# Performance work log

Measured on AMD Instinct MI355X. Metric: run time of the kernel, lower is better.

Reference implementation:

```python
import jax, jax.numpy as jnp
import numpy as np
import math

N_HEADS = 16
D_MODEL = 1024
D_FF = 4096
MAX_REL = 32  # max_relative_position
LN_EPS = 1e-5


def _layernorm(x, g, b):
    m = jnp.mean(x, axis=-1, keepdims=True)
    v = jnp.var(x, axis=-1, keepdims=True)
    return (x - m) * jax.lax.rsqrt(v + LN_EPS) * g + b


def setup_inputs() -> dict:
    key = jax.random.key(0)
    ks = jax.random.split(key, 12)
    D, F = D_MODEL, D_FF
    gain = 1.0 / math.sqrt(2.0)
    xav = lambda k, o, i, g=1.0: jax.random.uniform(k, (o, i), jnp.float32, -1.0, 1.0) * (g * math.sqrt(6.0 / (o + i)))
    return {
        "x": jax.random.normal(ks[0], (2, 2048, D), jnp.float32),
        "wq": xav(ks[1], D, D, gain),
        "wk": xav(ks[2], D, D, gain),
        "wv": xav(ks[3], D, D, gain),
        "wo": xav(ks[4], D, D, gain),
        "wo_b": jnp.zeros((D,), jnp.float32),
        "rel_tab": jax.random.normal(ks[5], (2 * MAX_REL - 1, N_HEADS), jnp.float32) * 0.02,
        "ln1_g": jnp.ones((D,), jnp.float32),
        "ln1_b": jnp.zeros((D,), jnp.float32),
        "ln2_g": jnp.ones((D,), jnp.float32),
        "ln2_b": jnp.zeros((D,), jnp.float32),
        "w1": xav(ks[6], F, D),
        "b1": jnp.zeros((F,), jnp.float32),
        "w2": xav(ks[7], D, F),
        "b2": jnp.zeros((D,), jnp.float32),
    }


def reference(x, wq, wk, wv, wo, wo_b, rel_tab, ln1_g, ln1_b, ln2_g, ln2_b, w1, b1, w2, b2):
    B, S, D = x.shape
    H = N_HEADS
    dk = D // H

    def proj(w):  # torch Linear: x @ w.T, then split heads -> [B,H,S,dk]
        return (x @ w.T).reshape(B, S, H, dk).transpose(0, 2, 1, 3)

    q, k, v = proj(wq), proj(wk), proj(wv)

    # Rotary embeddings (per-head dim), exact interleave-to-block formula from source
    t = jnp.arange(S, dtype=jnp.float32)
    inv_freq = 1.0 / (10000.0 ** (jnp.arange(0, dk, 2, dtype=jnp.float32) / dk))
    freqs = t[:, None] * inv_freq[None, :]  # [S, dk/2]
    cos, sin = jnp.cos(freqs), jnp.sin(freqs)

    def rope(z):
        z1, z2 = z[..., ::2], z[..., 1::2]  # [B,H,S,dk/2]
        return jnp.concatenate([z1 * cos - z2 * sin, z1 * sin + z2 * cos], axis=-1)

    q, k = rope(q), rope(k)

    # Manual attention with learned relative-position bias
    scores = jnp.einsum("bhqd,bhkd->bhqk", q, k) / math.sqrt(dk)
    rel = jnp.arange(S)[:, None] - jnp.arange(S)[None, :]
    rel = jnp.clip(rel, -(MAX_REL - 1), MAX_REL - 1) + (MAX_REL - 1)
    bias = rel_tab[rel]  # [S,S,H]
    scores = scores + jnp.transpose(bias, (2, 0, 1))[None]  # [1,H,S,S]
    attn = jax.nn.softmax(scores, axis=-1)
    o = jnp.einsum("bhqk,bhkd->bhqd", attn, v).transpose(0, 2, 1, 3).reshape(B, S, D)
    o = o @ wo.T + wo_b

    # Post-norm residual block
    h = _layernorm(x + o, ln1_g, ln1_b)
    f = jax.nn.gelu(h @ w1.T + b1, approximate=False) @ w2.T + b2
    return _layernorm(h + f, ln2_g, ln2_b)
```

## Files before the change

### kernel.cpp

```cpp
#include <hip/hip_runtime.h>
#include <stdint.h>

#define MB (1ull << 20)
typedef unsigned short u16;
typedef __attribute__((ext_vector_type(8))) short bf16x8;
typedef __attribute__((ext_vector_type(4))) float f32x4;

__device__ __forceinline__ float b2f(u16 u) {
  union { unsigned int i; float f; } c; c.i = ((unsigned int)u) << 16; return c.f;
}
__device__ __forceinline__ u16 f2b(float f) {
  union { float f; unsigned int i; } c; c.f = f;
  unsigned int r = c.i + 0x7fffu + ((c.i >> 16) & 1u);
  return (u16)(r >> 16);
}
__device__ __forceinline__ void gload16(const void* g, void* l) {
  __builtin_amdgcn_global_load_lds(
      (const __attribute__((address_space(1))) void*)g,
      (__attribute__((address_space(3))) void*)l, 16, 0, 0);
}

__global__ __launch_bounds__(256) void f2b_all(
    const float* __restrict__ x, const float* __restrict__ wq, const float* __restrict__ wk,
    const float* __restrict__ wv, const float* __restrict__ wo, const float* __restrict__ w1,
    const float* __restrict__ w2,
    u16* __restrict__ xb, u16* __restrict__ wqkvb, u16* __restrict__ wob,
    u16* __restrict__ w1b, u16* __restrict__ w2b)
{
  int bid = blockIdx.x;
  const float* src; u16* dst;
  if (bid < 4096)       { src = x;  dst = xb; }
  else if (bid < 5120)  { src = wq; dst = wqkvb;           bid -= 4096; }
  else if (bid < 6144)  { src = wk; dst = wqkvb + 1048576; bid -= 5120; }
  else if (bid < 7168)  { src = wv; dst = wqkvb + 2097152; bid -= 6144; }
  else if (bid < 8192)  { src = wo; dst = wob;             bid -= 7168; }
  else if (bid < 12288) { src = w1; dst = w1b;             bid -= 8192; }
  else                  { src = w2; dst = w2b;             bid -= 12288; }
  int i = (bid * 256 + threadIdx.x) * 4;
  float4 v = *(const float4*)(src + i);
  uint2 ov;
  ov.x = (unsigned)f2b(v.x) | ((unsigned)f2b(v.y) << 16);
  ov.y = (unsigned)f2b(v.z) | ((unsigned)f2b(v.w) << 16);
  *(uint2*)(dst + i) = ov;
}

__global__ __launch_bounds__(256) void rope_tab_kernel(float2* __restrict__ tab) {
  int idx = blockIdx.x * 256 + threadIdx.x;
  int s = idx >> 5, j = idx & 31;
  float inv = exp2f(-(float)j * (13.287712379549449f / 32.0f));
  float sn, cs;
  sincosf((float)s * inv, &sn, &cs);
  tab[idx] = make_float2(cs, sn);
}

template<int EPI, int BM>
__global__ __launch_bounds__(256) void gemm_bt(
    const u16* __restrict__ A, const u16* __restrict__ B,
    u16* __restrict__ C, const float* __restrict__ bias,
    int M, int N, int K)
{
  constexpr int MT = BM / 32;
  __shared__ __align__(16) u16 As[BM * 64];
  __shared__ __align__(16) u16 Bs[128 * 64];
  const int tid = threadIdx.x;
  const int lane = tid & 63, wave = tid >> 6;
  const int lr = lane & 15, lg = lane >> 4;
  const int wm = wave >> 1, wn = wave & 1;

  const int nwg = gridDim.x * gridDim.y;
  const int id = blockIdx.y * gridDim.x + blockIdx.x;
  const int nid = (id & 7) * (nwg >> 3) + (id >> 3);
  const int bx = nid % gridDim.x, by = nid / gridDim.x;

  const int srow = tid >> 3;
  const int scsw = ((tid & 7) * 8) ^ ((srow & 7) << 3);
  const size_t abase = (size_t)(by * BM + srow) * K + scsw;
  const size_t bbase = (size_t)(bx * 128 + srow) * K + scsw;

  int aoff[MT][2], boff[4][2];
  #pragma unroll
  for (int mt = 0; mt < MT; mt++) {
    int row = wm * (BM / 2) + mt * 16 + lr;
    #pragma unroll
    for (int kk = 0; kk < 2; kk++)
      aoff[mt][kk] = row * 64 + ((kk * 32 + lg * 8) ^ ((row & 7) << 3));
  }
  #pragma unroll
  for (int nt = 0; nt < 4; nt++) {
    int row = wn * 64 + nt * 16 + lr;
    #pragma unroll
    for (int kk = 0; kk < 2; kk++)
      boff[nt][kk] = row * 64 + ((kk * 32 + lg * 8) ^ ((row & 7) << 3));
  }

  f32x4 acc[MT][4];
  #pragma unroll
  for (int i = 0; i < MT; i++)
    #pragma unroll
    for (int j = 0; j < 4; j++) acc[i][j] = (f32x4){0.f, 0.f, 0.f, 0.f};

  for (int k0 = 0; k0 < K; k0 += 64) {
    __syncthreads();
    #pragma unroll
    for (int h = 0; h < MT; h++)
      gload16(A + abase + (size_t)(h * 32) * K + k0, &As[h * 2048 + tid * 8]);
    #pragma unroll
    for (int h = 0; h < 4; h++)
      gload16(B + bbase + (size_t)(h * 32) * K + k0, &Bs[h * 2048 + tid * 8]);
    __syncthreads();
    #pragma unroll
    for (int kk = 0; kk < 2; kk++) {
      bf16x8 af[MT], bfr[4];
      #pragma unroll
      for (int mt = 0; mt < MT; mt++) af[mt] = *(const bf16x8*)&As[aoff[mt][kk]];
      #pragma unroll
      for (int nt = 0; nt < 4; nt++) bfr[nt] = *(const bf16x8*)&Bs[boff[nt][kk]];
      #pragma unroll
      for (int mt = 0; mt < MT; mt++)
        #pragma unroll
        for (int nt = 0; nt < 4; nt++)
          acc[mt][nt] = __builtin_amdgcn_mfma_f32_16x16x32_bf16(af[mt], bfr[nt], acc[mt][nt], 0, 0, 0);
    }
  }

  #pragma unroll
  for (int mt = 0; mt < MT; mt++)
    #pragma unroll
    for (int nt = 0; nt < 4; nt++) {
      const int row = by * BM + wm * (BM / 2) + mt * 16 + lg * 4;
      const int col = bx * 128 + wn * 64 + nt * 16 + lr;
      const float bv = (EPI >= 1) ? bias[col] : 0.f;
      #pragma unroll
      for (int r = 0; r < 4; r++) {
        float x = acc[mt][nt][r] + bv;
        if (EPI == 2) x = 0.5f * x * (1.f + erff(x * 0.70710678118654752f));
        C[(size_t)(row + r) * N + col] = f2b(x);
      }
    }
}

#define MFMA16(BASE, BF)                                                       \
  __builtin_amdgcn_s_setprio(1);                                               \
  _Pragma("unroll")                                                            \
  for (int mt = 0; mt < 4; mt++)                                               \
    _Pragma("unroll")                                                          \
    for (int nt = 0; nt < 4; nt++)                                             \
      acc[(BASE) + mt][nt] = __builtin_amdgcn_mfma_f32_16x16x32_bf16(          \
          af[mt], BF[nt], acc[(BASE) + mt][nt], 0, 0, 0);                      \
  __builtin_amdgcn_s_setprio(0);

#define SA2(bb, eta, kb)                                                             \
  gload16(Ab + ((size_t)(eta) * 128) * K + (kb), &As[bb][eta][tid * 8]);             \
  gload16(Ab + ((size_t)(eta) * 128 + 64) * K + (kb), &As[bb][eta][4096 + tid * 8]);
#define SB2(bb, eta, kb)                                                             \
  gload16(Bb + ((size_t)(eta) * 128) * K + (kb), &Bs[bb][eta][tid * 8]);             \
  gload16(Bb + ((size_t)(eta) * 128 + 64) * K + (kb), &Bs[bb][eta][4096 + tid * 8]);

#define SBAR asm volatile("s_barrier" ::: "memory")

template<int EPI>
__global__ __launch_bounds__(512) void gemm256(
    const u16* __restrict__ A, const u16* __restrict__ B,
    u16* __restrict__ C, const float* __restrict__ bias,
    int M, int N, int K)
{
  __shared__ __align__(16) u16 As[2][2][8192];
  __shared__ __align__(16) u16 Bs[2][2][8192];
  const int tid = threadIdx.x;
  const int lane = tid & 63, wave = tid >> 6;
  const int lr = lane & 15, lg = lane >> 4;
  const int wm = wave >> 2, wn = wave & 3;

  const int nwg = gridDim.x * gridDim.y;
  const int id = blockIdx.y * gridDim.x + blockIdx.x;
  const int nid = (id & 7) * (nwg >> 3) + (id >> 3);
  const int bx = nid % gridDim.x, by = nid / gridDim.x;

  const int srow = tid >> 3;
  const int scsw = ((tid & 7) * 8) ^ ((srow & 7) << 3);
  const u16* Ab = A + (size_t)(by * 256 + srow) * K + scsw;
  const u16* Bb = B + (size_t)(bx * 256 + srow) * K + scsw;

  int aoff[2][2][4], boff[2][4];
  #pragma unroll
  for (int mh = 0; mh < 2; mh++)
    #pragma unroll
    for (int kk = 0; kk < 2; kk++)
      #pragma unroll
      for (int mt = 0; mt < 4; mt++) {
        int row = mh * 64 + mt * 16 + lr;
        aoff[mh][kk][mt] = row * 64 + ((kk * 32 + lg * 8) ^ ((lr & 7) << 3));
      }
  #pragma unroll
  for (int kk = 0; kk < 2; kk++)
    #pragma unroll
    for (int nt = 0; nt < 4; nt++) {
      int row = (wn & 1) * 64 + nt * 16 + lr;
      boff[kk][nt] = row * 64 + ((kk * 32 + lg * 8) ^ ((lr & 7) << 3));
    }

  f32x4 acc[8][4];
  #pragma unroll
  for (int i = 0; i < 8; i++)
    #pragma unroll
    for (int j = 0; j < 4; j++) acc[i][j] = (f32x4){0.f, 0.f, 0.f, 0.f};

  const int NT = K >> 6;

  SB2(0, 0, 0) SB2(0, 1, 0) SA2(0, 0, 0) SA2(0, 1, 0)

  for (int t = 0; t < NT; ++t) {
    const int c = t & 1, n = c ^ 1;
    const size_t kb = (size_t)(t + 1) * 64;
    const bool st = (t + 1 < NT);
    const u16* Ac = As[c][wm];
    const u16* Bc = Bs[c][wn >> 1];
    bf16x8 b0[4], b1[4], af[4];

    asm volatile("s_waitcnt vmcnt(0)" ::: "memory");
    SBAR;
    #pragma unroll
    for (int nt = 0; nt < 4; nt++) b0[nt] = *(const bf16x8*)&Bc[boff[0][nt]];
    #pragma unroll
    for (int mt = 0; mt < 4; mt++) af[mt] = *(const bf16x8*)&Ac[aoff[0][0][mt]];
    if (st) { SB2(n, 0, kb) }
    MFMA16(0, b0)
    SBAR;
    #pragma unroll
    for (int nt = 0; nt < 4; nt++) b1[nt] = *(const bf16x8*)&Bc[boff[1][nt]];
    #pragma unroll
    for (int mt = 0; mt < 4; mt++) af[mt] = *(const bf16x8*)&Ac[aoff[0][1][mt]];
    if (st) { SA2(n, 0, kb) }
    SBAR;
    MFMA16(0, b1)
    SBAR;
    #pragma unroll
    for (int mt = 0; mt < 4; mt++) af[mt] = *(const bf16x8*)&Ac[aoff[1][0][mt]];
    if (st) { SB2(n, 1, kb) }
    SBAR;
    MFMA16(4, b0)
    SBAR;
    #pragma unroll
    for (int mt = 0; mt < 4; mt++) af[mt] = *(const bf16x8*)&Ac[aoff[1][1][mt]];
    if (st) { SA2(n, 1, kb) }
    SBAR;
    MFMA16(4, b1)
    SBAR;
  }

  #pragma unroll
  for (int m8 = 0; m8 < 8; m8++)
    #pragma unroll
    for (int nt = 0; nt < 4; nt++) {
      const int row = by * 256 + wm * 128 + m8 * 16 + lg * 4;
      const int col = bx * 256 + wn * 64 + nt * 16 + lr;
      const float bv = (EPI >= 1) ? bias[col] : 0.f;
      #pragma unroll
      for (int r = 0; r < 4; r++) {
        float x = acc[m8][nt][r] + bv;
        if (EPI == 2) x = 0.5f * x * (1.f + erff(x * 0.70710678118654752f));
        C[(size_t)(row + r) * N + col] = f2b(x);
      }
    }
}

__global__ __launch_bounds__(256) void rope_kernel(
    const u16* __restrict__ qp, const u16* __restrict__ kp, int stride,
    const float2* __restrict__ tab, u16* __restrict__ qr, u16* __restrict__ kr)
{
  const int gid = blockIdx.x * 4 + (threadIdx.x >> 6);
  const int lane = threadIdx.x & 63;
  const int s = gid & 2047;
  const int bh = gid >> 11;
  const int h = bh & 15, b = bh >> 4;
  const int j = lane & 31;
  float2 t = tab[s * 32 + j];
  const float cs = t.x, sn = t.y;
  const size_t base = (size_t)(b * 2048 + s) * stride + h * 64;
  unsigned int qv = *(const unsigned int*)(qp + base + 2 * j);
  unsigned int kv = *(const unsigned int*)(kp + base + 2 * j);
  float q1 = b2f((u16)qv), q2 = b2f((u16)(qv >> 16));
  float k1 = b2f((u16)kv), k2 = b2f((u16)(kv >> 16));
  float qo = (lane < 32) ? (q1 * cs - q2 * sn) : (q1 * sn + q2 * cs);
  float ko = (lane < 32) ? (k1 * cs - k2 * sn) : (k1 * sn + k2 * cs);
  qr[(size_t)gid * 64 + lane] = f2b(qo * 0.18033688011112042f);
  kr[(size_t)gid * 64 + lane] = f2b(ko);
}

__global__ __launch_bounds__(256) void vtrans_kernel(
    const u16* __restrict__ vp, int stride, u16* __restrict__ vT)
{
  __shared__ u16 t[64][65];
  const int sc = blockIdx.x & 31;
  const int bh = blockIdx.x >> 5;
  const int h = bh & 15, b = bh >> 4;
  const int tid = threadIdx.x;
  #pragma unroll
  for (int i = 0; i < 16; i++) {
    int idx = i * 256 + tid;
    int sl = idx >> 6, d = idx & 63;
    t[sl][d] = vp[(size_t)(b * 2048 + sc * 64 + sl) * stride + h * 64 + d];
  }
  __syncthreads();
  #pragma unroll
  for (int i = 0; i < 16; i++) {
    int idx = i * 256 + tid;
    int d = idx >> 6, sl = idx & 63;
    vT[((size_t)bh * 64 + d) * 2048 + sc * 64 + sl] = t[sl][d];
  }
}

__global__ __launch_bounds__(256) void attn_kernel(
    const u16* __restrict__ qr, const u16* __restrict__ kr,
    const u16* __restrict__ vT, const float* __restrict__ rel_tab,
    u16* __restrict__ o)
{
  __shared__ __align__(16) u16 Ks[2][64 * 64];
  __shared__ __align__(16) u16 Vs[2][64 * 64];
  __shared__ float bias_s[64];

  const int tid = threadIdx.x;
  const int lane = tid & 63, wave = tid >> 6;
  const int lr = lane & 15, lg = lane >> 4;

  const int id = blockIdx.x;
  const int nid = (id & 7) * 128 + (id >> 3);
  const int bh = nid >> 5, qc = nid & 31;
  const int h = bh & 15, b = bh >> 4;
  const int q0 = qc * 64 + wave * 16;

  if (tid < 63) bias_s[tid] = rel_tab[tid * 16 + h] * 1.4426950408889634f;

  const u16* qb = qr + (size_t)bh * 2048 * 64;
  const u16* kb = kr + (size_t)bh * 2048 * 64;
  const u16* vb = vT + (size_t)bh * 64 * 2048;

  bf16x8 qf[2];
  qf[0] = *(const bf16x8*)(qb + (size_t)(q0 + lr) * 64 + lg * 8);
  qf[1] = *(const bf16x8*)(qb + (size_t)(q0 + lr) * 64 + 32 + lg * 8);

  const int srow = tid >> 3;
  const int scsw = ((tid & 7) * 8) ^ ((srow & 7) << 3);

  int koff[4][2];
  #pragma unroll
  for (int nt = 0; nt < 4; nt++)
    #pragma unroll
    for (int ks = 0; ks < 2; ks++)
      koff[nt][ks] = (nt * 16 + lr) * 64 + ((ks * 32 + lg * 8) ^ ((lr & 7) << 3));

  #pragma unroll
  for (int hh = 0; hh < 2; hh++) {
    gload16(kb + (size_t)(hh * 32 + srow) * 64 + scsw, &Ks[0][hh * 2048 + tid * 8]);
    gload16(vb + (size_t)(hh * 32 + srow) * 2048 + scsw, &Vs[0][hh * 2048 + tid * 8]);
  }

  float mrow = -1e30f;
  f32x4 lvec = (f32x4){0.f, 0.f, 0.f, 0.f};
  f32x4 oacc[4];
  #pragma unroll
  for (int nt = 0; nt < 4; nt++) oacc[nt] = (f32x4){0.f, 0.f, 0.f, 0.f};

  const int idx_lo = 4 * (lr + 16 * ((lg & 1) * 2));
  const int idx_hi = idx_lo + 64;
  const bool hiSel = (lg >= 2);

  int cur = 0;
  for (int kc = 0; kc < 32; kc++) {
    const int k0 = kc * 64;
    __syncthreads();
    if (kc < 31) {
      const int kn = k0 + 64;
      #pragma unroll
      for (int hh = 0; hh < 2; hh++) {
        gload16(kb + (size_t)(kn + hh * 32 + srow) * 64 + scsw, &Ks[cur ^ 1][hh * 2048 + tid * 8]);
        gload16(vb + (size_t)(hh * 32 + srow) * 2048 + kn + scsw, &Vs[cur ^ 1][hh * 2048 + tid * 8]);
      }
    }
    const u16* Kc = Ks[cur];
    const u16* Vc = Vs[cur];

    f32x4 sacc[4];
    #pragma unroll
    for (int nt = 0; nt < 4; nt++) sacc[nt] = (f32x4){0.f, 0.f, 0.f, 0.f};
    __builtin_amdgcn_s_setprio(1);
    #pragma unroll
    for (int ks = 0; ks < 2; ks++)
      #pragma unroll
      for (int nt = 0; nt < 4; nt++) {
        bf16x8 kf = *(const bf16x8*)&Kc[koff[nt][ks]];
        sacc[nt] = __builtin_amdgcn_mfma_f32_16x16x32_bf16(kf, qf[ks], sacc[nt], 0, 0, 0);
      }
    __builtin_amdgcn_s_setprio(0);

    f32x4 pvv[4];
    const int dmin = q0 - k0 - 63, dmax = q0 + 15 - k0;
    if (dmin >= 31 || dmax <= -31) {
      const float c = bias_s[dmin >= 31 ? 62 : 0];
      f32x4 m4;
      #pragma unroll
      for (int i = 0; i < 4; i++)
        m4[i] = fmaxf(fmaxf(sacc[0][i], sacc[1][i]), fmaxf(sacc[2][i], sacc[3][i]));
      float rm = fmaxf(fmaxf(m4[0], m4[1]), fmaxf(m4[2], m4[3])) + c;
      rm = fmaxf(rm, __shfl_xor(rm, 16));
      rm = fmaxf(rm, __shfl_xor(rm, 32));
      if (!__all(rm <= mrow + 11.5f)) {
        float mnew = fmaxf(mrow, rm);
        float sc = exp2f(mrow - mnew);
        lvec *= sc;
        #pragma unroll
        for (int nt = 0; nt < 4; nt++) oacc[nt] *= sc;
        mrow = mnew;
      }
      const float off = c - mrow;
      #pragma unroll
      for (int nt = 0; nt < 4; nt++) pvv[nt] = sacc[nt] + off;
    } else {
      #pragma unroll
      for (int nt = 0; nt < 4; nt++)
        #pragma unroll
        for (int r = 0; r < 4; r++) {
          int d = (q0 + lr) - (k0 + nt * 16 + lg * 4 + r);
          d = d < -31 ? -31 : (d > 31 ? 31 : d);
          pvv[nt][r] = sacc[nt][r] + bias_s[d + 31];
        }
      f32x4 m4;
      #pragma unroll
      for (int i = 0; i < 4; i++)
        m4[i] = fmaxf(fmaxf(pvv[0][i], pvv[1][i]), fmaxf(pvv[2][i], pvv[3][i]));
      float rm = fmaxf(fmaxf(m4[0], m4[1]), fmaxf(m4[2], m4[3]));
      rm = fmaxf(rm, __shfl_xor(rm, 16));
      rm = fmaxf(rm, __shfl_xor(rm, 32));
      if (!__all(rm <= mrow + 11.5f)) {
        float mnew = fmaxf(mrow, rm);
        float sc = exp2f(mrow - mnew);
        lvec *= sc;
        #pragma unroll
        for (int nt = 0; nt < 4; nt++) oacc[nt] *= sc;
        mrow = mnew;
      }
      #pragma unroll
      for (int nt = 0; nt < 4; nt++) pvv[nt] = pvv[nt] - mrow;
    }

    unsigned int pk[4][2];
    #pragma unroll
    for (int nt = 0; nt < 4; nt++) {
      f32x4 p;
      #pragma unroll
      for (int i = 0; i < 4; i++) p[i] = exp2f(pvv[nt][i]);
      lvec += p;
      unsigned int pr0, pr1;
      asm("v_cvt_pk_bf16_f32 %0, %1, %2" : "=v"(pr0) : "v"(p[0]), "v"(p[1]));
      asm("v_cvt_pk_bf16_f32 %0, %1, %2" : "=v"(pr1) : "v"(p[2]), "v"(p[3]));
      pk[nt][0] = pr0;
      pk[nt][1] = pr1;
    }

    __builtin_amdgcn_s_setprio(1);
    #pragma unroll
    for (int ks = 0; ks < 2; ks++) {
      int w0a = __builtin_amdgcn_ds_bpermute(idx_lo, (int)pk[ks * 2][0]);
      int w0b = __builtin_amdgcn_ds_bpermute(idx_lo, (int)pk[ks * 2 + 1][0]);
      int w1a = __builtin_amdgcn_ds_bpermute(idx_lo, (int)pk[ks * 2][1]);
      int w1b = __builtin_amdgcn_ds_bpermute(idx_lo, (int)pk[ks * 2 + 1][1]);
      int w2a = __builtin_amdgcn_ds_bpermute(idx_hi, (int)pk[ks * 2][0]);
      int w2b = __builtin_amdgcn_ds_bpermute(idx_hi, (int)pk[ks * 2 + 1][0]);
      int w3a = __builtin_amdgcn_ds_bpermute(idx_hi, (int)pk[ks * 2][1]);
      int w3b = __builtin_amdgcn_ds_bpermute(idx_hi, (int)pk[ks * 2 + 1][1]);
      int4 bw;
      bw.x = hiSel ? w0b : w0a;
      bw.y = hiSel ? w1b : w1a;
      bw.z = hiSel ? w2b : w2a;
      bw.w = hiSel ? w3b : w3a;
      bf16x8 pf = *(bf16x8*)&bw;
      #pragma unroll
      for (int nt = 0; nt < 4; nt++) {
        bf16x8 vf = *(const bf16x8*)&Vc[koff[nt][ks]];
        oacc[nt] = __builtin_amdgcn_mfma_f32_16x16x32_bf16(vf, pf, oacc[nt], 0, 0, 0);
      }
    }
    __builtin_amdgcn_s_setprio(0);
    cur ^= 1;
  }

  float lpart = (lvec[0] + lvec[1]) + (lvec[2] + lvec[3]);
  lpart += __shfl_xor(lpart, 16);
  lpart += __shfl_xor(lpart, 32);
  const float inv = 1.0f / lpart;
  const size_t obase = (size_t)(b * 2048 + q0 + lr) * 1024 + h * 64;
  #pragma unroll
  for (int nt = 0; nt < 4; nt++) {
    uint2 st;
    st.x = (unsigned)f2b(oacc[nt][0] * inv) | ((unsigned)f2b(oacc[nt][1] * inv) << 16);
    st.y = (unsigned)f2b(oacc[nt][2] * inv) | ((unsigned)f2b(oacc[nt][3] * inv) << 16);
    *(uint2*)(o + obase + nt * 16 + lg * 4) = st;
  }
}

__global__ __launch_bounds__(256) void ln1_kernel(
    const float* __restrict__ x, const u16* __restrict__ ao,
    const float* __restrict__ g, const float* __restrict__ bta,
    u16* __restrict__ hb)
{
  const int row = blockIdx.x, tid = threadIdx.x;
  const int wave = tid >> 6, lane = tid & 63;
  const int c = tid * 4;
  float4 xv = *(const float4*)(x + (size_t)row * 1024 + c);
  uint2 av = *(const uint2*)(ao + (size_t)row * 1024 + c);
  float v0 = xv.x + b2f((u16)av.x);
  float v1 = xv.y + b2f((u16)(av.x >> 16));
  float v2 = xv.z + b2f((u16)av.y);
  float v3 = xv.w + b2f((u16)(av.y >> 16));
  float s = (v0 + v1) + (v2 + v3);
  float s2 = (v0 * v0 + v1 * v1) + (v2 * v2 + v3 * v3);
  #pragma unroll
  for (int off = 32; off >= 1; off >>= 1) { s += __shfl_down(s, off); s2 += __shfl_down(s2, off); }
  __shared__ float rs[4], rs2[4];
  if (lane == 0) { rs[wave] = s; rs2[wave] = s2; }
  __syncthreads();
  s = rs[0] + rs[1] + rs[2] + rs[3];
  s2 = rs2[0] + rs2[1] + rs2[2] + rs2[3];
  float mean = s * (1.f / 1024.f);
  float var = s2 * (1.f / 1024.f) - mean * mean;
  float inv = rsqrtf(var + 1e-5f);
  float4 gv = *(const float4*)(g + c);
  float4 bv = *(const float4*)(bta + c);
  uint2 ov;
  ov.x = (unsigned)f2b((v0 - mean) * inv * gv.x + bv.x) |
         ((unsigned)f2b((v1 - mean) * inv * gv.y + bv.y) << 16);
  ov.y = (unsigned)f2b((v2 - mean) * inv * gv.z + bv.z) |
         ((unsigned)f2b((v3 - mean) * inv * gv.w + bv.w) << 16);
  *(uint2*)(hb + (size_t)row * 1024 + c) = ov;
}

__global__ __launch_bounds__(256) void ln2_kernel(
    const u16* __restrict__ hb, const u16* __restrict__ fb,
    const float* __restrict__ g, const float* __restrict__ bta,
    float* __restrict__ out)
{
  const int row = blockIdx.x, tid = threadIdx.x;
  const int wave = tid >> 6, lane = tid & 63;
  const int c = tid * 4;
  uint2 hv = *(const uint2*)(hb + (size_t)row * 1024 + c);
  uint2 fv = *(const uint2*)(fb + (size_t)row * 1024 + c);
  float v0 = b2f((u16)hv.x) + b2f((u16)fv.x);
  float v1 = b2f((u16)(hv.x >> 16)) + b2f((u16)(fv.x >> 16));
  float v2 = b2f((u16)hv.y) + b2f((u16)fv.y);
  float v3 = b2f((u16)(hv.y >> 16)) + b2f((u16)(fv.y >> 16));
  float s = (v0 + v1) + (v2 + v3);
  float s2 = (v0 * v0 + v1 * v1) + (v2 * v2 + v3 * v3);
  #pragma unroll
  for (int off = 32; off >= 1; off >>= 1) { s += __shfl_down(s, off); s2 += __shfl_down(s2, off); }
  __shared__ float rs[4], rs2[4];
  if (lane == 0) { rs[wave] = s; rs2[wave] = s2; }
  __syncthreads();
  s = rs[0] + rs[1] + rs[2] + rs[3];
  s2 = rs2[0] + rs2[1] + rs2[2] + rs2[3];
  float mean = s * (1.f / 1024.f);
  float var = s2 * (1.f / 1024.f) - mean * mean;
  float inv = rsqrtf(var + 1e-5f);
  float4 gv = *(const float4*)(g + c);
  float4 bv = *(const float4*)(bta + c);
  float4 ov;
  ov.x = (v0 - mean) * inv * gv.x + bv.x;
  ov.y = (v1 - mean) * inv * gv.y + bv.y;
  ov.z = (v2 - mean) * inv * gv.z + bv.z;
  ov.w = (v3 - mean) * inv * gv.w + bv.w;
  *(float4*)(out + (size_t)row * 1024 + c) = ov;
}

extern "C" void kernel_launch(void* const* d_in, const int* in_sizes, int n_in,
                              void* d_out, int out_size, void* d_ws, size_t ws_size,
                              hipStream_t stream)
{
  const float* x    = (const float*)d_in[0];
  const float* wq   = (const float*)d_in[1];
  const float* wk   = (const float*)d_in[2];
  const float* wv   = (const float*)d_in[3];
  const float* wo   = (const float*)d_in[4];
  const float* wo_b = (const float*)d_in[5];
  const float* rel  = (const float*)d_in[6];
  const float* ln1g = (const float*)d_in[7];
  const float* ln1b = (const float*)d_in[8];
  const float* ln2g = (const float*)d_in[9];
  const float* ln2b = (const float*)d_in[10];
  const float* w1   = (const float*)d_in[11];
  const float* b1   = (const float*)d_in[12];
  const float* w2   = (const float*)d_in[13];
  const float* b2   = (const float*)d_in[14];
  float* out = (float*)d_out;
  char* w = (char*)d_ws;

  if (ws_size < (size_t)90 * MB) return;

  u16* xb    = (u16*)(w + 0 * MB);
  u16* wqkvb = (u16*)(w + 8 * MB);
  u16* wob   = (u16*)(w + 14 * MB);
  u16* w1b   = (u16*)(w + 16 * MB);
  u16* w2b   = (u16*)(w + 24 * MB);
  u16* qkv   = (u16*)(w + 32 * MB);
  u16* ob    = (u16*)(w + 32 * MB);
  u16* ao    = (u16*)(w + 40 * MB);
  u16* hb    = (u16*)(w + 48 * MB);
  u16* qrb   = (u16*)(w + 56 * MB);
  u16* krb   = (u16*)(w + 64 * MB);
  u16* vTb   = (u16*)(w + 72 * MB);
  u16* gb    = (u16*)(w + 56 * MB);
  u16* fb    = (u16*)(w + 0 * MB);
  float2* tab = (float2*)(w + 88 * MB);

  const int M = 4096, D = 1024, F = 4096;

  rope_tab_kernel<<<dim3(256), 256, 0, stream>>>(tab);
  f2b_all<<<dim3(16384), 256, 0, stream>>>(x, wq, wk, wv, wo, w1, w2,
                                           xb, wqkvb, wob, w1b, w2b);

  gemm256<0><<<dim3(3 * D / 256, M / 256), 512, 0, stream>>>(xb, wqkvb, qkv, nullptr, M, 3 * D, D);

  rope_kernel<<<dim3(16384), 256, 0, stream>>>(qkv, qkv + 1024, 3 * D, tab, qrb, krb);
  vtrans_kernel<<<dim3(1024), 256, 0, stream>>>(qkv + 2048, 3 * D, vTb);

  attn_kernel<<<dim3(1024), 256, 0, stream>>>(qrb, krb, vTb, rel, ob);

  gemm_bt<1, 64><<<dim3(D / 128, M / 64), 256, 0, stream>>>(ob, wob, ao, wo_b, M, D, D);

  ln1_kernel<<<dim3(M), 256, 0, stream>>>(x, ao, ln1g, ln1b, hb);

  gemm256<2><<<dim3(F / 256, M / 256), 512, 0, stream>>>(hb, w1b, gb, b1, M, F, D);

  gemm_bt<1, 64><<<dim3(D / 128, M / 64), 256, 0, stream>>>(gb, w2b, fb, b2, M, D, F);

  ln2_kernel<<<dim3(M), 256, 0, stream>>>(hb, fb, ln2g, ln2b, out);
}
```

Measured before the change: 289.6 us.

## Process two 16-row query tiles per wave in attention to reuse K/V tiles

Each attention block now handles 128 query rows instead of 64: every wave keeps two independent Q fragments and two sets of softmax state and accumulators. Each K/V tile loaded into LDS then feeds twice as many MFMAs, and the grid shrinks from 1024 to 512 blocks. This halves global K/V traffic and LDS fill per query and gives more independent MFMA work to interleave. The cost is roughly double the accumulator registers, which may lower occupancy, and 512 blocks may underfill the GPU's compute units.

Result: slower. 298.0 us (+2.9%).

```diff
diff --git a/kernel.cpp b/kernel.cpp
--- a/kernel.cpp
+++ b/kernel.cpp
@@ -324,10 +324,11 @@
   const int lr = lane & 15, lg = lane >> 4;
 
   const int id = blockIdx.x;
-  const int nid = (id & 7) * 128 + (id >> 3);
-  const int bh = nid >> 5, qc = nid & 31;
+  const int nid = (id & 7) * 64 + (id >> 3);
+  const int bh = nid >> 4, qc = nid & 15;
   const int h = bh & 15, b = bh >> 4;
-  const int q0 = qc * 64 + wave * 16;
+  const int q0a = qc * 128 + wave * 16;
+  const int q0b = q0a + 64;
 
   if (tid < 63) bias_s[tid] = rel_tab[tid * 16 + h] * 1.4426950408889634f;
 
@@ -335,9 +336,11 @@
   const u16* kb = kr + (size_t)bh * 2048 * 64;
   const u16* vb = vT + (size_t)bh * 64 * 2048;
 
-  bf16x8 qf[2];
-  qf[0] = *(const bf16x8*)(qb + (size_t)(q0 + lr) * 64 + lg * 8);
-  qf[1] = *(const bf16x8*)(qb + (size_t)(q0 + lr) * 64 + 32 + lg * 8);
+  bf16x8 qfa[2], qfb[2];
+  qfa[0] = *(const bf16x8*)(qb + (size_t)(q0a + lr) * 64 + lg * 8);
+  qfa[1] = *(const bf16x8*)(qb + (size_t)(q0a + lr) * 64 + 32 + lg * 8);
+  qfb[0] = *(const bf16x8*)(qb + (size_t)(q0b + lr) * 64 + lg * 8);
+  qfb[1] = *(const bf16x8*)(qb + (size_t)(q0b + lr) * 64 + 32 + lg * 8);
 
   const int srow = tid >> 3;
   const int scsw = ((tid & 7) * 8) ^ ((srow & 7) << 3);
@@ -355,44 +358,22 @@
     gload16(vb + (size_t)(hh * 32 + srow) * 2048 + scsw, &Vs[0][hh * 2048 + tid * 8]);
   }
 
-  float mrow = -1e30f;
-  f32x4 lvec = (f32x4){0.f, 0.f, 0.f, 0.f};
-  f32x4 oacc[4];
-  #pragma unroll
-  for (int nt = 0; nt < 4; nt++) oacc[nt] = (f32x4){0.f, 0.f, 0.f, 0.f};
+  float mrow_a = -1e30f, mrow_b = -1e30f;
+  f32x4 lvec_a = (f32x4){0.f, 0.f, 0.f, 0.f};
+  f32x4 lvec_b = (f32x4){0.f, 0.f, 0.f, 0.f};
+  f32x4 oacc_a[4], oacc_b[4];
+  #pragma unroll
+  for (int nt = 0; nt < 4; nt++) {
+    oacc_a[nt] = (f32x4){0.f, 0.f, 0.f, 0.f};
+    oacc_b[nt] = (f32x4){0.f, 0.f, 0.f, 0.f};
+  }
 
   const int idx_lo = 4 * (lr + 16 * ((lg & 1) * 2));
   const int idx_hi = idx_lo + 64;
   const bool hiSel = (lg >= 2);
 
-  int cur = 0;
-  for (int kc = 0; kc < 32; kc++) {
-    const int k0 = kc * 64;
-    __syncthreads();
-    if (kc < 31) {
-      const int kn = k0 + 64;
-      #pragma unroll
-      for (int hh = 0; hh < 2; hh++) {
-        gload16(kb + (size_t)(kn + hh * 32 + srow) * 64 + scsw, &Ks[cur ^ 1][hh * 2048 + tid * 8]);
-        gload16(vb + (size_t)(hh * 32 + srow) * 2048 + kn + scsw, &Vs[cur ^ 1][hh * 2048 + tid * 8]);
-      }
-    }
-    const u16* Kc = Ks[cur];
-    const u16* Vc = Vs[cur];
-
-    f32x4 sacc[4];
-    #pragma unroll
-    for (int nt = 0; nt < 4; nt++) sacc[nt] = (f32x4){0.f, 0.f, 0.f, 0.f};
-    __builtin_amdgcn_s_setprio(1);
-    #pragma unroll
-    for (int ks = 0; ks < 2; ks++)
-      #pragma unroll
-      for (int nt = 0; nt < 4; nt++) {
-        bf16x8 kf = *(const bf16x8*)&Kc[koff[nt][ks]];
-        sacc[nt] = __builtin_amdgcn_mfma_f32_16x16x32_bf16(kf, qf[ks], sacc[nt], 0, 0, 0);
-      }
-    __builtin_amdgcn_s_setprio(0);
-
+  auto softmax = [&](f32x4 sacc[4], float& mrow, f32x4& lvec, f32x4 oacc[4],
+                     int q0, int k0, unsigned int pk[4][2]) {
     f32x4 pvv[4];
     const int dmin = q0 - k0 - 63, dmax = q0 + 15 - k0;
     if (dmin >= 31 || dmax <= -31) {
@@ -442,8 +423,6 @@
       #pragma unroll
       for (int nt = 0; nt < 4; nt++) pvv[nt] = pvv[nt] - mrow;
     }
-
-    unsigned int pk[4][2];
     #pragma unroll
     for (int nt = 0; nt < 4; nt++) {
       f32x4 p;
@@ -456,45 +435,95 @@
       pk[nt][0] = pr0;
       pk[nt][1] = pr1;
     }
-
+  };
+
+  auto exchange = [&](const unsigned int pk[4][2], int ks) -> bf16x8 {
+    int w0a = __builtin_amdgcn_ds_bpermute(idx_lo, (int)pk[ks * 2][0]);
+    int w0b = __builtin_amdgcn_ds_bpermute(idx_lo, (int)pk[ks * 2 + 1][0]);
+    int w1a = __builtin_amdgcn_ds_bpermute(idx_lo, (int)pk[ks * 2][1]);
+    int w1b = __builtin_amdgcn_ds_bpermute(idx_lo, (int)pk[ks * 2 + 1][1]);
+    int w2a = __builtin_amdgcn_ds_bpermute(idx_hi, (int)pk[ks * 2][0]);
+    int w2b = __builtin_amdgcn_ds_bpermute(idx_hi, (int)pk[ks * 2 + 1][0]);
+    int w3a = __builtin_amdgcn_ds_bpermute(idx_hi, (int)pk[ks * 2][1]);
+    int w3b = __builtin_amdgcn_ds_bpermute(idx_hi, (int)pk[ks * 2 + 1][1]);
+    int4 bw;
+    bw.x = hiSel ? w0b : w0a;
+    bw.y = hiSel ? w1b : w1a;
+    bw.z = hiSel ? w2b : w2a;
+    bw.w = hiSel ? w3b : w3a;
+    return *(bf16x8*)&bw;
+  };
+
+  int cur = 0;
+  for (int kc = 0; kc < 32; kc++) {
+    const int k0 = kc * 64;
+    __syncthreads();
+    if (kc < 31) {
+      const int kn = k0 + 64;
+      #pragma unroll
+      for (int hh = 0; hh < 2; hh++) {
+        gload16(kb + (size_t)(kn + hh * 32 + srow) * 64 + scsw, &Ks[cur ^ 1][hh * 2048 + tid * 8]);
+        gload16(vb + (size_t)(hh * 32 + srow) * 2048 + kn + scsw, &Vs[cur ^ 1][hh * 2048 + tid * 8]);
+      }
+    }
+    const u16* Kc = Ks[cur];
+    const u16* Vc = Vs[cur];
+
+    f32x4 sacc_a[4], sacc_b[4];
+    #pragma unroll
+    for (int nt = 0; nt < 4; nt++) {
+      sacc_a[nt] = (f32x4){0.f, 0.f, 0.f, 0.f};
+      sacc_b[nt] = (f32x4){0.f, 0.f, 0.f, 0.f};
+    }
     __builtin_amdgcn_s_setprio(1);
     #pragma unroll
+    for (int ks = 0; ks < 2; ks++)
+      #pragma unroll
+      for (int nt = 0; nt < 4; nt++) {
+        bf16x8 kf = *(const bf16x8*)&Kc[koff[nt][ks]];
+        sacc_a[nt] = __builtin_amdgcn_mfma_f32_16x16x32_bf16(kf, qfa[ks], sacc_a[nt], 0, 0, 0);
+        sacc_b[nt] = __builtin_amdgcn_mfma_f32_16x16x32_bf16(kf, qfb[ks], sacc_b[nt], 0, 0, 0);
+      }
+    __builtin_amdgcn_s_setprio(0);
+
+    unsigned int pk_a[4][2], pk_b[4][2];
+    softmax(sacc_a, mrow_a, lvec_a, oacc_a, q0a, k0, pk_a);
+    softmax(sacc_b, mrow_b, lvec_b, oacc_b, q0b, k0, pk_b);
+
+    __builtin_amdgcn_s_setprio(1);
+    #pragma unroll
     for (int ks = 0; ks < 2; ks++) {
-      int w0a = __builtin_amdgcn_ds_bpermute(idx_lo, (int)pk[ks * 2][0]);
-      int w0b = __builtin_amdgcn_ds_bpermute(idx_lo, (int)pk[ks * 2 + 1][0]);
-      int w1a = __builtin_amdgcn_ds_bpermute(idx_lo, (int)pk[ks * 2][1]);
-      int w1b = __builtin_amdgcn_ds_bpermute(idx_lo, (int)pk[ks * 2 + 1][1]);
-      int w2a = __builtin_amdgcn_ds_bpermute(idx_hi, (int)pk[ks * 2][0]);
-      int w2b = __builtin_amdgcn_ds_bpermute(idx_hi, (int)pk[ks * 2 + 1][0]);
-      int w3a = __builtin_amdgcn_ds_bpermute(idx_hi, (int)pk[ks * 2][1]);
-      int w3b = __builtin_amdgcn_ds_bpermute(idx_hi, (int)pk[ks * 2 + 1][1]);
-      int4 bw;
-      bw.x = hiSel ? w0b : w0a;
-      bw.y = hiSel ? w1b : w1a;
-      bw.z = hiSel ? w2b : w2a;
-      bw.w = hiSel ? w3b : w3a;
-      bf16x8 pf = *(bf16x8*)&bw;
+      bf16x8 pfa = exchange(pk_a, ks);
+      bf16x8 pfb = exchange(pk_b, ks);
       #pragma unroll
       for (int nt = 0; nt < 4; nt++) {
         bf16x8 vf = *(const bf16x8*)&Vc[koff[nt][ks]];
-        oacc[nt] = __builtin_amdgcn_mfma_f32_16x16x32_bf16(vf, pf, oacc[nt], 0, 0, 0);
+        oacc_a[nt] = __builtin_amdgcn_mfma_f32_16x16x32_bf16(vf, pfa, oacc_a[nt], 0, 0, 0);
+        oacc_b[nt] = __builtin_amdgcn_mfma_f32_16x16x32_bf16(vf, pfb, oacc_b[nt], 0, 0, 0);
       }
     }
     __builtin_amdgcn_s_setprio(0);
     cur ^= 1;
   }
 
-  float lpart = (lvec[0] + lvec[1]) + (lvec[2] + lvec[3]);
-  lpart += __shfl_xor(lpart, 16);
-  lpart += __shfl_xor(lpart, 32);
-  const float inv = 1.0f / lpart;
-  const size_t obase = (size_t)(b * 2048 + q0 + lr) * 1024 + h * 64;
+  float la = (lvec_a[0] + lvec_a[1]) + (lvec_a[2] + lvec_a[3]);
+  la += __shfl_xor(la, 16);
+  la += __shfl_xor(la, 32);
+  float lb = (lvec_b[0] + lvec_b[1]) + (lvec_b[2] + lvec_b[3]);
+  lb += __shfl_xor(lb, 16);
+  lb += __shfl_xor(lb, 32);
+  const float inva = 1.0f / la, invb = 1.0f / lb;
+  const size_t obase_a = (size_t)(b * 2048 + q0a + lr) * 1024 + h * 64;
+  const size_t obase_b = (size_t)(b * 2048 + q0b + lr) * 1024 + h * 64;
   #pragma unroll
   for (int nt = 0; nt < 4; nt++) {
     uint2 st;
-    st.x = (unsigned)f2b(oacc[nt][0] * inv) | ((unsigned)f2b(oacc[nt][1] * inv) << 16);
-    st.y = (unsigned)f2b(oacc[nt][2] * inv) | ((unsigned)f2b(oacc[nt][3] * inv) << 16);
-    *(uint2*)(o + obase + nt * 16 + lg * 4) = st;
+    st.x = (unsigned)f2b(oacc_a[nt][0] * inva) | ((unsigned)f2b(oacc_a[nt][1] * inva) << 16);
+    st.y = (unsigned)f2b(oacc_a[nt][2] * inva) | ((unsigned)f2b(oacc_a[nt][3] * inva) << 16);
+    *(uint2*)(o + obase_a + nt * 16 + lg * 4) = st;
+    st.x = (unsigned)f2b(oacc_b[nt][0] * invb) | ((unsigned)f2b(oacc_b[nt][1] * invb) << 16);
+    st.y = (unsigned)f2b(oacc_b[nt][2] * invb) | ((unsigned)f2b(oacc_b[nt][3] * invb) << 16);
+    *(uint2*)(o + obase_b + nt * 16 + lg * 4) = st;
   }
 }
 
@@ -621,7 +650,7 @@
   rope_kernel<<<dim3(16384), 256, 0, stream>>>(qkv, qkv + 1024, 3 * D, tab, qrb, krb);
   vtrans_kernel<<<dim3(1024), 256, 0, stream>>>(qkv + 2048, 3 * D, vTb);
 
-  attn_kernel<<<dim3(1024), 256, 0, stream>>>(qrb, krb, vTb, rel, ob);
+  attn_kernel<<<dim3(512), 256, 0, stream>>>(qrb, krb, vTb, rel, ob);
 
   gemm_bt<1, 64><<<dim3(D / 128, M / 64), 256, 0, stream>>>(ob, wob, ao, wo_b, M, D, D);
 
```

## Split-K the two N=1024 GEMMs and reduce partials in layernorm kernels

Applied to the files above, without the earlier changes.

The output-projection and FFN-down GEMMs now split K in two and launch twice as many workgroups, each writing a bf16 partial result to its own buffer. The ln1/ln2 kernels sum the two partials and add the bias that the GEMM epilogue used to apply. The aim is to fill more CUs on these narrow N=1024 GEMMs, which had only 512 workgroups. The cost is extra partial-buffer traffic and an added bf16 rounding step on each partial. Buffers are remapped so hb moves to offset 32MB, reusing the ob region, which is consumed before ln1 writes hb.

After: 275.8 us. 4.8% less time.

```diff
diff --git a/kernel.cpp b/kernel.cpp
--- a/kernel.cpp
+++ b/kernel.cpp
@@ -53,13 +53,11 @@
   tab[idx] = make_float2(cs, sn);
 }
 
-template<int EPI, int BM>
-__global__ __launch_bounds__(256) void gemm_bt(
+__global__ __launch_bounds__(256) void gemm_ks(
     const u16* __restrict__ A, const u16* __restrict__ B,
-    u16* __restrict__ C, const float* __restrict__ bias,
-    int M, int N, int K)
-{
-  constexpr int MT = BM / 32;
+    u16* __restrict__ C, int M, int N, int K)
+{
+  constexpr int BM = 64, MT = 2;
   __shared__ __align__(16) u16 As[BM * 64];
   __shared__ __align__(16) u16 Bs[128 * 64];
   const int tid = threadIdx.x;
@@ -70,12 +68,16 @@
   const int nwg = gridDim.x * gridDim.y;
   const int id = blockIdx.y * gridDim.x + blockIdx.x;
   const int nid = (id & 7) * (nwg >> 3) + (id >> 3);
-  const int bx = nid % gridDim.x, by = nid / gridDim.x;
+  const int bx = nid % gridDim.x, byk = nid / gridDim.x;
+  const int kslice = byk & 1, by = byk >> 1;
+  const int Kh = K >> 1;
+  const int kofs = kslice * Kh;
+  u16* Cs = C + (size_t)kslice * M * N;
 
   const int srow = tid >> 3;
   const int scsw = ((tid & 7) * 8) ^ ((srow & 7) << 3);
-  const size_t abase = (size_t)(by * BM + srow) * K + scsw;
-  const size_t bbase = (size_t)(bx * 128 + srow) * K + scsw;
+  const size_t abase = (size_t)(by * BM + srow) * K + kofs + scsw;
+  const size_t bbase = (size_t)(bx * 128 + srow) * K + kofs + scsw;
 
   int aoff[MT][2], boff[4][2];
   #pragma unroll
@@ -99,7 +101,7 @@
     #pragma unroll
     for (int j = 0; j < 4; j++) acc[i][j] = (f32x4){0.f, 0.f, 0.f, 0.f};
 
-  for (int k0 = 0; k0 < K; k0 += 64) {
+  for (int k0 = 0; k0 < Kh; k0 += 64) {
     __syncthreads();
     #pragma unroll
     for (int h = 0; h < MT; h++)
@@ -129,13 +131,9 @@
     for (int nt = 0; nt < 4; nt++) {
       const int row = by * BM + wm * (BM / 2) + mt * 16 + lg * 4;
       const int col = bx * 128 + wn * 64 + nt * 16 + lr;
-      const float bv = (EPI >= 1) ? bias[col] : 0.f;
-      #pragma unroll
-      for (int r = 0; r < 4; r++) {
-        float x = acc[mt][nt][r] + bv;
-        if (EPI == 2) x = 0.5f * x * (1.f + erff(x * 0.70710678118654752f));
-        C[(size_t)(row + r) * N + col] = f2b(x);
-      }
+      #pragma unroll
+      for (int r = 0; r < 4; r++)
+        Cs[(size_t)(row + r) * N + col] = f2b(acc[mt][nt][r]);
     }
 }
 
@@ -499,7 +497,8 @@
 }
 
 __global__ __launch_bounds__(256) void ln1_kernel(
-    const float* __restrict__ x, const u16* __restrict__ ao,
+    const float* __restrict__ x, const u16* __restrict__ ao0,
+    const u16* __restrict__ ao1, const float* __restrict__ wob,
     const float* __restrict__ g, const float* __restrict__ bta,
     u16* __restrict__ hb)
 {
@@ -507,11 +506,13 @@
   const int wave = tid >> 6, lane = tid & 63;
   const int c = tid * 4;
   float4 xv = *(const float4*)(x + (size_t)row * 1024 + c);
-  uint2 av = *(const uint2*)(ao + (size_t)row * 1024 + c);
-  float v0 = xv.x + b2f((u16)av.x);
-  float v1 = xv.y + b2f((u16)(av.x >> 16));
-  float v2 = xv.z + b2f((u16)av.y);
-  float v3 = xv.w + b2f((u16)(av.y >> 16));
+  uint2 a0 = *(const uint2*)(ao0 + (size_t)row * 1024 + c);
+  uint2 a1 = *(const uint2*)(ao1 + (size_t)row * 1024 + c);
+  float4 wb = *(const float4*)(wob + c);
+  float v0 = xv.x + b2f((u16)a0.x) + b2f((u16)a1.x) + wb.x;
+  float v1 = xv.y + b2f((u16)(a0.x >> 16)) + b2f((u16)(a1.x >> 16)) + wb.y;
+  float v2 = xv.z + b2f((u16)a0.y) + b2f((u16)a1.y) + wb.z;
+  float v3 = xv.w + b2f((u16)(a0.y >> 16)) + b2f((u16)(a1.y >> 16)) + wb.w;
   float s = (v0 + v1) + (v2 + v3);
   float s2 = (v0 * v0 + v1 * v1) + (v2 * v2 + v3 * v3);
   #pragma unroll
@@ -535,7 +536,8 @@
 }
 
 __global__ __launch_bounds__(256) void ln2_kernel(
-    const u16* __restrict__ hb, const u16* __restrict__ fb,
+    const u16* __restrict__ hb, const u16* __restrict__ fb0,
+    const u16* __restrict__ fb1, const float* __restrict__ b2,
     const float* __restrict__ g, const float* __restrict__ bta,
     float* __restrict__ out)
 {
@@ -543,11 +545,13 @@
   const int wave = tid >> 6, lane = tid & 63;
   const int c = tid * 4;
   uint2 hv = *(const uint2*)(hb + (size_t)row * 1024 + c);
-  uint2 fv = *(const uint2*)(fb + (size_t)row * 1024 + c);
-  float v0 = b2f((u16)hv.x) + b2f((u16)fv.x);
-  float v1 = b2f((u16)(hv.x >> 16)) + b2f((u16)(fv.x >> 16));
-  float v2 = b2f((u16)hv.y) + b2f((u16)fv.y);
-  float v3 = b2f((u16)(hv.y >> 16)) + b2f((u16)(fv.y >> 16));
+  uint2 f0 = *(const uint2*)(fb0 + (size_t)row * 1024 + c);
+  uint2 f1 = *(const uint2*)(fb1 + (size_t)row * 1024 + c);
+  float4 b2v = *(const float4*)(b2 + c);
+  float v0 = b2f((u16)hv.x) + b2f((u16)f0.x) + b2f((u16)f1.x) + b2v.x;
+  float v1 = b2f((u16)(hv.x >> 16)) + b2f((u16)(f0.x >> 16)) + b2f((u16)(f1.x >> 16)) + b2v.y;
+  float v2 = b2f((u16)hv.y) + b2f((u16)f0.y) + b2f((u16)f1.y) + b2v.z;
+  float v3 = b2f((u16)(hv.y >> 16)) + b2f((u16)(f0.y >> 16)) + b2f((u16)(f1.y >> 16)) + b2v.w;
   float s = (v0 + v1) + (v2 + v3);
   float s2 = (v0 * v0 + v1 * v1) + (v2 * v2 + v3 * v3);
   #pragma unroll
@@ -601,13 +605,13 @@
   u16* w2b   = (u16*)(w + 24 * MB);
   u16* qkv   = (u16*)(w + 32 * MB);
   u16* ob    = (u16*)(w + 32 * MB);
-  u16* ao    = (u16*)(w + 40 * MB);
-  u16* hb    = (u16*)(w + 48 * MB);
+  u16* ao01  = (u16*)(w + 40 * MB);
+  u16* hb    = (u16*)(w + 32 * MB);
   u16* qrb   = (u16*)(w + 56 * MB);
   u16* krb   = (u16*)(w + 64 * MB);
   u16* vTb   = (u16*)(w + 72 * MB);
   u16* gb    = (u16*)(w + 56 * MB);
-  u16* fb    = (u16*)(w + 0 * MB);
+  u16* fb01  = (u16*)(w + 0 * MB);
   float2* tab = (float2*)(w + 88 * MB);
 
   const int M = 4096, D = 1024, F = 4096;
@@ -623,13 +627,15 @@
 
   attn_kernel<<<dim3(1024), 256, 0, stream>>>(qrb, krb, vTb, rel, ob);
 
-  gemm_bt<1, 64><<<dim3(D / 128, M / 64), 256, 0, stream>>>(ob, wob, ao, wo_b, M, D, D);
-
-  ln1_kernel<<<dim3(M), 256, 0, stream>>>(x, ao, ln1g, ln1b, hb);
+  gemm_ks<<<dim3(D / 128, (M / 64) * 2), 256, 0, stream>>>(ob, wob, ao01, M, D, D);
+
+  ln1_kernel<<<dim3(M), 256, 0, stream>>>(x, ao01, ao01 + (size_t)M * D, wo_b,
+                                          ln1g, ln1b, hb);
 
   gemm256<2><<<dim3(F / 256, M / 256), 512, 0, stream>>>(hb, w1b, gb, b1, M, F, D);
 
-  gemm_bt<1, 64><<<dim3(D / 128, M / 64), 256, 0, stream>>>(gb, w2b, fb, b2, M, D, F);
-
-  ln2_kernel<<<dim3(M), 256, 0, stream>>>(hb, fb, ln2g, ln2b, out);
-}
+  gemm_ks<<<dim3(D / 128, (M / 64) * 2), 256, 0, stream>>>(gb, w2b, fb01, M, D, F);
+
+  ln2_kernel<<<dim3(M), 256, 0, stream>>>(hb, fb01, fb01 + (size_t)M * D, b2,
+                                          ln2g, ln2b, out);
+}
```
